# Performance work log

Hardware: AMD Instinct MI355X
Metric: run time of the kernel (lower is better)

Reference implementation:

```python
import jax, jax.numpy as jnp
import numpy as np

B, D, H, Z, E = 2048, 1024, 1024, 256, 64


def setup_inputs() -> dict:
    key = jax.random.key(0)
    ks = jax.random.split(key, 16)
    s = lambda k, shape, std=0.02: jax.random.normal(k, shape, dtype=jnp.float32) * std
    return {
        "x": jax.random.normal(ks[0], (B, D), dtype=jnp.float32),
        "h0": jax.random.normal(ks[1], (B, H), dtype=jnp.float32),
        "c0": jax.random.normal(ks[2], (B, H), dtype=jnp.float32),
        "hhat0": jax.random.normal(ks[3], (B, Z), dtype=jnp.float32),
        "chat0": jax.random.normal(ks[4], (B, Z), dtype=jnp.float32),
        "hweight": s(ks[5], (Z + H + D, 4 * Z)),
        "hbias": jnp.zeros((4 * Z,), jnp.float32),
        "zweight_h": s(ks[6], (Z, 4 * E), 0.01),
        "zweight_x": s(ks[7], (Z, 4 * E), 0.01),
        "zweight_b": s(ks[8], (Z, 4 * E), 0.01),
        "zbias_h": jnp.ones((4 * E,), jnp.float32),
        "zbias_x": jnp.ones((4 * E,), jnp.float32),
        # stacked in gate order (i, g, f, o), matching the torch cat order
        "dweight_h": jnp.full((4, E, H), 0.1 / E, jnp.float32),
        "dweight_x": jnp.full((4, E, H), 0.1 / E, jnp.float32),
        "dweight_b": s(ks[9], (4, E, H), 0.01),
        "weight": s(ks[10], (H + D, 4 * H)),
        "bias": jnp.zeros((4 * H,), jnp.float32),
    }


def reference(x, h0, c0, hhat0, chat0, hweight, hbias,
              zweight_h, zweight_x, zweight_b, zbias_h, zbias_x,
              dweight_h, dweight_x, dweight_b, weight, bias):
    # ---- hyper LSTM cell ----
    hcat = jnp.concatenate([hhat0, h0, x], axis=1)                 # [B, Z+H+D]
    hg = hcat @ hweight + hbias                                    # [B, 4Z]
    i_h, g_h, f_h, o_h = jnp.split(hg, 4, axis=1)
    chat1 = jax.nn.sigmoid(f_h) * chat0 + jax.nn.sigmoid(i_h) * jnp.tanh(g_h)
    hhat1 = jax.nn.sigmoid(o_h) * jnp.tanh(chat1)                  # [B, Z]

    # ---- embeddings z (gate order i, g, f, o) ----
    z_h = (hhat1 @ zweight_h + zbias_h).reshape(-1, 4, E)          # [B,4,E]
    z_x = (hhat1 @ zweight_x + zbias_x).reshape(-1, 4, E)
    z_b = (hhat1 @ zweight_b).reshape(-1, 4, E)

    # ---- per-gate modulation vectors d_y* : [B,4,H] -> [B,4H] ----
    d_yh = jnp.einsum('bge,geh->bgh', z_h, dweight_h).reshape(-1, 4 * H)
    d_yx = jnp.einsum('bge,geh->bgh', z_x, dweight_x).reshape(-1, 4 * H)
    d_yb = jnp.einsum('bge,geh->bgh', z_b, dweight_b).reshape(-1, 4 * H)

    # ---- main LSTM with hypernetwork modulation ----
    gates = jnp.concatenate([h0, x], axis=1) @ weight              # [B, 4H]
    gates = gates * d_yh * d_yx + d_yb + bias
    i_g, g_g, f_g, o_g = jnp.split(gates, 4, axis=1)
    c1 = jax.nn.sigmoid(f_g) * c0 + jax.nn.sigmoid(i_g) * jnp.tanh(g_g)
    h1 = jax.nn.sigmoid(o_g) * jnp.tanh(c1)
    return (h1, c1, hhat1, chat1)
```

## Files before the change

### kernel.cpp

```cpp
#include <hip/hip_runtime.h>
#include <hip/hip_bf16.h>
#include <math.h>


typedef __attribute__((ext_vector_type(8))) short bf16x8;
typedef __attribute__((ext_vector_type(4))) float f32x4;
typedef unsigned short u16;

__device__ __forceinline__ u16 f2b(float f) {
  union { float f; unsigned u; } v; v.f = f;
  unsigned r = v.u + 0x7fffu + ((v.u >> 16) & 1u);
  return (u16)(r >> 16);
}
__device__ __forceinline__ float b2f(u16 b) {
  union { unsigned u; float f; } v; v.u = ((unsigned)b) << 16; return v.f;
}
__device__ __forceinline__ float sigm(float x) { return 1.f / (1.f + __expf(-x)); }

#define GLL16(gsrc, ldst)                                                      \
  __builtin_amdgcn_global_load_lds(                                            \
      (const __attribute__((address_space(1))) void*)(gsrc),                   \
      (__attribute__((address_space(3))) void*)(ldst), 16, 0, 0)

__global__ void k_prep(const float* __restrict__ hhat0, const float* __restrict__ h0,
                       const float* __restrict__ x, const float* __restrict__ weight,
                       const float* __restrict__ hweight,
                       const float* __restrict__ zw_h, const float* __restrict__ zw_x,
                       const float* __restrict__ zw_b, const float* __restrict__ dw_h,
                       const float* __restrict__ dw_x, const float* __restrict__ dw_b,
                       u16* __restrict__ hcatb, u16* __restrict__ bt,
                       u16* __restrict__ zwT, u16* __restrict__ dwT) {
  __shared__ float tile[32][66];
  int bid = blockIdx.x;
  const int t = threadIdx.x;
  if (bid < 4608) {
    int i = bid * 256 + t;
    int b = i / 576, c4 = i % 576;
    const float* src;
    if (c4 < 64)       src = hhat0 + (long)b * 256 + c4 * 4;
    else if (c4 < 320) src = h0 + (long)b * 1024 + (c4 - 64) * 4;
    else               src = x + (long)b * 1024 + (c4 - 320) * 4;
    float4 v = *(const float4*)src;
    ushort4 o = {f2b(v.x), f2b(v.y), f2b(v.z), f2b(v.w)};
    *(ushort4*)&hcatb[(long)b * 2304 + c4 * 4] = o;
    return;
  }
  bid -= 4608;
  if (bid < 5760) {
    const int n0 = (bid % 160) * 32, k0 = (bid / 160) * 64;
    if (n0 < 4096 && k0 < 256) return;
    const float* src; int C, sc0, sr0;
    if (n0 >= 4096) { src = hweight; C = 1024; sc0 = n0 - 4096; sr0 = k0; }
    else            { src = weight;  C = 4096; sc0 = n0;        sr0 = k0 - 256; }
    #pragma unroll
    for (int p = 0; p < 8; ++p) {
      int c = t & 31, r = (t >> 5) + 8 * p;
      tile[c][r] = src[(long)(sr0 + r) * C + sc0 + c];
    }
    __syncthreads();
    #pragma unroll
    for (int p = 0; p < 2; ++p) {
      int kc = t & 15, cl = (t >> 4) + 16 * p;
      ushort4 o = {f2b(tile[cl][4 * kc]), f2b(tile[cl][4 * kc + 1]),
                   f2b(tile[cl][4 * kc + 2]), f2b(tile[cl][4 * kc + 3])};
      *(ushort4*)&bt[(long)(n0 + cl) * 2304 + k0 + 4 * kc] = o;
    }
    return;
  }
  bid -= 5760;
  const int zi = bid >> 5, bx = bid & 31;
  const float* src; u16* dst; int R, C;
  if (zi < 3) {
    src = (zi == 0) ? zw_h : (zi == 1) ? zw_x : zw_b;
    dst = zwT + (long)zi * 65536; R = 256; C = 256;
  } else {
    int s = zi - 3, tt = s >> 2, g = s & 3;
    src = ((tt == 0) ? dw_h : (tt == 1) ? dw_x : dw_b) + (long)g * 65536;
    dst = dwT + (long)s * 65536; R = 64; C = 1024;
  }
  const int nct = C / 32;
  const int c0 = (bx % nct) * 32, r0 = (bx / nct) * 64;
  #pragma unroll
  for (int p = 0; p < 8; ++p) {
    int c = t & 31, r = (t >> 5) + 8 * p;
    tile[c][r] = src[(long)(r0 + r) * C + c0 + c];
  }
  __syncthreads();
  #pragma unroll
  for (int p = 0; p < 2; ++p) {
    int kc = t & 15, cl = (t >> 4) + 16 * p;
    ushort4 o = {f2b(tile[cl][4 * kc]), f2b(tile[cl][4 * kc + 1]),
                 f2b(tile[cl][4 * kc + 2]), f2b(tile[cl][4 * kc + 3])};
    *(ushort4*)&dst[(long)(c0 + cl) * R + r0 + 4 * kc] = o;
  }
}

__global__ __launch_bounds__(512, 4)
void k_gemm_main(const u16* __restrict__ A, const u16* __restrict__ Bt,
                 float* __restrict__ hgbuf, u16* __restrict__ grawb) {
  constexpr int K = 2304, BK = 32;
  __shared__ __align__(16) u16 sA[128 * BK];
  __shared__ __align__(16) u16 sB[128 * BK];
  const int m0 = blockIdx.y * 128, n0 = blockIdx.x * 128;
  const int kstart = (n0 < 4096) ? 256 : 0;
  const int tid = threadIdx.x, wave = tid >> 6, lane = tid & 63;
  const int quad = lane >> 4, lrow = lane & 15;
  const int wm = (wave >> 2) * 64, wn = (wave & 3) * 32;

  const int sl = tid * 16;
  const int srow = sl >> 6;
  const int sq = (((sl & 63) >> 4) - (srow >> 1)) & 3;
  const long aoff = ((long)(m0 + srow) * K) * 2 + sq * 16;
  const long boff = ((long)(n0 + srow) * K) * 2 + sq * 16;

  const f32x4 vz = {0.f, 0.f, 0.f, 0.f};
  f32x4 acc[4][2];
  #pragma unroll
  for (int i = 0; i < 4; ++i)
    #pragma unroll
    for (int j = 0; j < 2; ++j) acc[i][j] = vz;

  for (int k0 = kstart; k0 < K; k0 += BK) {
    GLL16((const char*)A + aoff + (long)k0 * 2, (char*)sA + wave * 1024);
    GLL16((const char*)Bt + boff + (long)k0 * 2, (char*)sB + wave * 1024);
    __syncthreads();
    bf16x8 af[4], bf[2];
    #pragma unroll
    for (int i = 0; i < 4; ++i) {
      int row = wm + i * 16 + lrow;
      af[i] = *(const bf16x8*)((const char*)sA + row * 64 + (((quad + (row >> 1)) & 3) << 4));
    }
    #pragma unroll
    for (int j = 0; j < 2; ++j) {
      int row = wn + j * 16 + lrow;
      bf[j] = *(const bf16x8*)((const char*)sB + row * 64 + (((quad + (row >> 1)) & 3) << 4));
    }
    #pragma unroll
    for (int i = 0; i < 4; ++i)
      #pragma unroll
      for (int j = 0; j < 2; ++j)
        acc[i][j] = __builtin_amdgcn_mfma_f32_16x16x32_bf16(af[i], bf[j], acc[i][j], 0, 0, 0);
    __syncthreads();
  }
  #pragma unroll
  for (int i = 0; i < 4; ++i) {
    #pragma unroll
    for (int j = 0; j < 2; ++j) {
      #pragma unroll
      for (int r = 0; r < 4; ++r) {
        int row = m0 + wm + i * 16 + quad * 4 + r;
        int col = n0 + wn + j * 16 + lrow;
        float v = acc[i][j][r];
        if (col < 4096) grawb[(long)row * 4096 + col] = f2b(v);
        else            hgbuf[(long)row * 1024 + (col - 4096)] = v;
      }
    }
  }
}

__global__ __launch_bounds__(256, 2)
void k_gemm_z(const u16* __restrict__ A, const u16* __restrict__ Bt,
              const float* __restrict__ zbh, const float* __restrict__ zbx,
              u16* __restrict__ zbout) {
  constexpr int K = 256, BK = 32;
  __shared__ __align__(16) u16 sA[64 * BK];
  __shared__ __align__(16) u16 sB[128 * BK];
  const int m0 = blockIdx.y * 64, n0 = blockIdx.x * 128;
  const int tid = threadIdx.x, wave = tid >> 6, lane = tid & 63;
  const int quad = lane >> 4, lrow = lane & 15;
  const int wm = (wave >> 1) * 32, wn = (wave & 1) * 64;

  const int sl = tid * 16;
  const int arow = sl >> 6;
  const int aq = (((sl & 63) >> 4) - (arow >> 1)) & 3;
  const long aoff = ((long)(m0 + arow) * K) * 2 + aq * 16;

  const f32x4 vz = {0.f, 0.f, 0.f, 0.f};
  f32x4 acc[2][4];
  #pragma unroll
  for (int i = 0; i < 2; ++i)
    #pragma unroll
    for (int j = 0; j < 4; ++j) acc[i][j] = vz;

  for (int k0 = 0; k0 < K; k0 += BK) {
    GLL16((const char*)A + aoff + (long)k0 * 2, (char*)sA + wave * 1024);
    #pragma unroll
    for (int c = 0; c < 2; ++c) {
      int l = c * 4096 + sl;
      int row = l >> 6;
      int q = (((l & 63) >> 4) - (row >> 1)) & 3;
      const char* g = (const char*)Bt + ((long)(n0 + row) * K + k0) * 2 + q * 16;
      GLL16(g, (char*)sB + c * 4096 + wave * 1024);
    }
    __syncthreads();
    bf16x8 af[2], bf[4];
    #pragma unroll
    for (int i = 0; i < 2; ++i) {
      int row = wm + i * 16 + lrow;
      af[i] = *(const bf16x8*)((const char*)sA + row * 64 + (((quad + (row >> 1)) & 3) << 4));
    }
    #pragma unroll
    for (int j = 0; j < 4; ++j) {
      int row = wn + j * 16 + lrow;
      bf[j] = *(const bf16x8*)((const char*)sB + row * 64 + (((quad + (row >> 1)) & 3) << 4));
    }
    #pragma unroll
    for (int i = 0; i < 2; ++i)
      #pragma unroll
      for (int j = 0; j < 4; ++j)
        acc[i][j] = __builtin_amdgcn_mfma_f32_16x16x32_bf16(af[i], bf[j], acc[i][j], 0, 0, 0);
    __syncthreads();
  }
  #pragma unroll
  for (int i = 0; i < 2; ++i) {
    #pragma unroll
    for (int j = 0; j < 4; ++j) {
      #pragma unroll
      for (int r = 0; r < 4; ++r) {
        int row = m0 + wm + i * 16 + quad * 4 + r;
        int col = n0 + wn + j * 16 + lrow;
        float v = acc[i][j][r] + ((col < 256) ? zbh[col] : (col < 512) ? zbx[col - 256] : 0.f);
        zbout[(long)row * 768 + col] = f2b(v);
      }
    }
  }
}

__global__ void k_hyper_act(const float* __restrict__ hgbuf, const float* __restrict__ hbias,
                            const float* __restrict__ chat0,
                            float* __restrict__ chat1, float* __restrict__ hhat1,
                            u16* __restrict__ hhat1b) {
  int idx = blockIdx.x * 256 + threadIdx.x;
  int b = idx >> 8, zc = idx & 255;
  const float* row = hgbuf + (long)b * 1024;
  float ih = row[zc] + hbias[zc];
  float gh = row[256 + zc] + hbias[256 + zc];
  float fh = row[512 + zc] + hbias[512 + zc];
  float oh = row[768 + zc] + hbias[768 + zc];
  float c = sigm(fh) * chat0[idx] + sigm(ih) * tanhf(gh);
  float h = sigm(oh) * tanhf(c);
  chat1[idx] = c;
  hhat1[idx] = h;
  hhat1b[idx] = f2b(h);
}

__global__ __launch_bounds__(256, 2)
void k_dmod_lstm(const u16* __restrict__ z, const u16* __restrict__ dwT,
                 const u16* __restrict__ grawb, const float* __restrict__ bias,
                 const float* __restrict__ c0, float* __restrict__ h1,
                 float* __restrict__ c1) {
  __shared__ __align__(16) u16 sZ[64 * 192];
  __shared__ __align__(16) u16 sW[3 * 64 * 64];
  const int m0 = blockIdx.y * 64;
  const int hc0 = blockIdx.x * 64;
  const int tid = threadIdx.x, wave = tid >> 6, lane = tid & 63;
  const int quad = lane >> 4, lrow = lane & 15;
  const int wm = (wave >> 1) * 32, wn = (wave & 1) * 32;
  const f32x4 vz4 = {0.f, 0.f, 0.f, 0.f};

  f32x4 pcar[2][2];
  f32x4 ccar[2][2];

  #pragma unroll
  for (int g = 0; g < 4; ++g) {
    #pragma unroll
    for (int c = 0; c < 6; ++c) {
      int l = c * 4096 + tid * 16;
      int ci = l >> 4, row = ci / 24, p = ci - row * 24;
      int q = p + 72 - row; q -= (q / 24) * 24;
      int tt = q >> 3, e16 = q & 7;
      const char* gz = (const char*)z + (long)(m0 + row) * 1536 + tt * 512 + g * 128 + e16 * 16;
      GLL16(gz, (char*)sZ + c * 4096 + wave * 1024);
      int t2 = l >> 13, rw = (l & 8191) >> 7, p2 = (l >> 4) & 7;
      int q2 = (p2 - rw) & 7;
      const char* gw = (const char*)dwT + (long)((t2 * 4 + g) * 1024 + hc0 + rw) * 128 + q2 * 16;
      GLL16(gw, (char*)sW + c * 4096 + wave * 1024);
    }
    __syncthreads();
    f32x4 aH[2][2], aX[2][2], aB[2][2];
    #pragma unroll
    for (int i = 0; i < 2; ++i)
      #pragma unroll
      for (int j = 0; j < 2; ++j) { aH[i][j] = vz4; aX[i][j] = vz4; aB[i][j] = vz4; }
    #pragma unroll
    for (int kk = 0; kk < 2; ++kk) {
      bf16x8 za[3][2], wb[3][2];
      #pragma unroll
      for (int t = 0; t < 3; ++t) {
        #pragma unroll
        for (int i = 0; i < 2; ++i) {
          int row = wm + i * 16 + lrow;
          int q0 = t * 8 + kk * 4 + quad;
          int ph = q0 + row; ph -= (ph / 24) * 24;
          za[t][i] = *(const bf16x8*)((const char*)sZ + row * 384 + ph * 16);
        }
        #pragma unroll
        for (int j = 0; j < 2; ++j) {
          int row = wn + j * 16 + lrow;
          int q0 = kk * 4 + quad;
          int ph = (q0 + row) & 7;
          wb[t][j] = *(const bf16x8*)((const char*)sW + t * 8192 + row * 128 + ph * 16);
        }
      }
      #pragma unroll
      for (int i = 0; i < 2; ++i)
        #pragma unroll
        for (int j = 0; j < 2; ++j) {
          aH[i][j] = __builtin_amdgcn_mfma_f32_16x16x32_bf16(za[0][i], wb[0][j], aH[i][j], 0, 0, 0);
          aX[i][j] = __builtin_amdgcn_mfma_f32_16x16x32_bf16(za[1][i], wb[1][j], aX[i][j], 0, 0, 0);
          aB[i][j] = __builtin_amdgcn_mfma_f32_16x16x32_bf16(za[2][i], wb[2][j], aB[i][j], 0, 0, 0);
        }
    }
    __syncthreads();
    #pragma unroll
    for (int i = 0; i < 2; ++i) {
      #pragma unroll
      for (int j = 0; j < 2; ++j) {
        #pragma unroll
        for (int r = 0; r < 4; ++r) {
          int row = m0 + wm + i * 16 + quad * 4 + r;
          int col = wn + j * 16 + lrow;
          float gr = b2f(grawb[(long)row * 4096 + g * 1024 + hc0 + col]);
          float v = gr * aH[i][j][r] * aX[i][j][r] + aB[i][j][r] + bias[g * 1024 + hc0 + col];
          long idx = (long)row * 1024 + hc0 + col;
          if (g == 0) pcar[i][j][r] = sigm(v);
          else if (g == 1) pcar[i][j][r] *= tanhf(v);
          else if (g == 2) {
            float cc = sigm(v) * c0[idx] + pcar[i][j][r];
            ccar[i][j][r] = cc;
            c1[idx] = cc;
          } else {
            h1[idx] = sigm(v) * tanhf(ccar[i][j][r]);
          }
        }
      }
    }
  }
}


extern "C" void kernel_launch(void* const* d_in, const int* in_sizes, int n_in,
                              void* d_out, int out_size, void* d_ws, size_t ws_size,
                              hipStream_t stream) {
  const float* x      = (const float*)d_in[0];
  const float* h0     = (const float*)d_in[1];
  const float* c0     = (const float*)d_in[2];
  const float* hhat0  = (const float*)d_in[3];
  const float* chat0  = (const float*)d_in[4];
  const float* hweight= (const float*)d_in[5];
  const float* hbias  = (const float*)d_in[6];
  const float* zw_h   = (const float*)d_in[7];
  const float* zw_x   = (const float*)d_in[8];
  const float* zw_b   = (const float*)d_in[9];
  const float* zb_h   = (const float*)d_in[10];
  const float* zb_x   = (const float*)d_in[11];
  const float* dw_h   = (const float*)d_in[12];
  const float* dw_x   = (const float*)d_in[13];
  const float* dw_b   = (const float*)d_in[14];
  const float* weight = (const float*)d_in[15];
  const float* bias   = (const float*)d_in[16];
  float* out = (float*)d_out;

  char* w = (char*)d_ws;
  auto take = [&](size_t bytes) { char* p = w; w += (bytes + 255) & ~(size_t)255; return p; };
  u16*   hcatb  = (u16*)take(2048ull * 2304 * 2);
  u16*   btc    = (u16*)take(5120ull * 2304 * 2);
  u16*   zwT    = (u16*)take(768ull * 256 * 2);
  u16*   dwT    = (u16*)take(12ull * 1024 * 64 * 2);
  u16*   grawb  = (u16*)take(2048ull * 4096 * 2);
  float* hgbuf  = (float*)take(2048ull * 1024 * 4);
  u16*   hhat1b = (u16*)take(2048ull * 256 * 2);
  u16*   zb16   = (u16*)take(2048ull * 768 * 2);

  float* h1_o    = out;
  float* c1_o    = out + 2048 * 1024;
  float* hhat1_o = out + 2 * 2048 * 1024;
  float* chat1_o = out + 2 * 2048 * 1024 + 2048 * 256;

  k_prep<<<4608 + 5760 + 480, 256, 0, stream>>>(
      hhat0, h0, x, weight, hweight, zw_h, zw_x, zw_b, dw_h, dw_x, dw_b,
      hcatb, btc, zwT, dwT);

  k_gemm_main<<<dim3(40, 16), 512, 0, stream>>>(hcatb, btc, hgbuf, grawb);

  k_hyper_act<<<2048, 256, 0, stream>>>(hgbuf, hbias, chat0, chat1_o, hhat1_o, hhat1b);

  k_gemm_z<<<dim3(6, 32), 256, 0, stream>>>(hhat1b, zwT, zb_h, zb_x, zb16);

  k_dmod_lstm<<<dim3(16, 32), 256, 0, stream>>>(zb16, dwT, grawb, bias, c0, h1_o, c1_o);
}
```

Before: 230.8 us.

## Widen main GEMM K-tile, fuse hyper cell into z GEMM, drop LDS in dmod

The main GEMM now stages a 64-wide K slice per iteration with an 8-way XOR swizzle, which halves the number of barrier-separated loop trips. The hyper-LSTM activation kernel is folded into the z GEMM: each block computes hhat1 for its 64 rows straight into LDS, so the separate launch and the bf16 hhat1 round trip go away. Six column blocks each recompute the same rows, which duplicates the transcendental work. The dmod/LSTM kernel no longer stages z and dW through shared memory and loads MFMA operands directly from global memory, removing barriers but relying on cache hits for reuse.

After: 273.3 us. +18.4%, slower.

```diff
diff --git a/kernel.cpp b/kernel.cpp
--- a/kernel.cpp
+++ b/kernel.cpp
@@ -98,20 +98,23 @@
 __global__ __launch_bounds__(512, 4)
 void k_gemm_main(const u16* __restrict__ A, const u16* __restrict__ Bt,
                  float* __restrict__ hgbuf, u16* __restrict__ grawb) {
-  constexpr int K = 2304, BK = 32;
-  __shared__ __align__(16) u16 sA[128 * BK];
-  __shared__ __align__(16) u16 sB[128 * BK];
+  constexpr int K = 2304;
+  __shared__ __align__(16) u16 sA[128 * 64];
+  __shared__ __align__(16) u16 sB[128 * 64];
   const int m0 = blockIdx.y * 128, n0 = blockIdx.x * 128;
   const int kstart = (n0 < 4096) ? 256 : 0;
   const int tid = threadIdx.x, wave = tid >> 6, lane = tid & 63;
   const int quad = lane >> 4, lrow = lane & 15;
   const int wm = (wave >> 2) * 64, wn = (wave & 3) * 32;
 
-  const int sl = tid * 16;
-  const int srow = sl >> 6;
-  const int sq = (((sl & 63) >> 4) - (srow >> 1)) & 3;
-  const long aoff = ((long)(m0 + srow) * K) * 2 + sq * 16;
-  const long boff = ((long)(n0 + srow) * K) * 2 + sq * 16;
+  const int l0 = tid * 16, l1 = 8192 + tid * 16;
+  const int r0 = l0 >> 7, r1 = l1 >> 7;
+  const int q0 = (((l0 >> 4) & 7) - r0) & 7;
+  const int q1 = (((l1 >> 4) & 7) - r1) & 7;
+  const long aoff0 = ((long)(m0 + r0) * K + q0 * 8) * 2;
+  const long aoff1 = ((long)(m0 + r1) * K + q1 * 8) * 2;
+  const long boff0 = ((long)(n0 + r0) * K + q0 * 8) * 2;
+  const long boff1 = ((long)(n0 + r1) * K + q1 * 8) * 2;
 
   const f32x4 vz = {0.f, 0.f, 0.f, 0.f};
   f32x4 acc[4][2];
@@ -120,26 +123,34 @@
     #pragma unroll
     for (int j = 0; j < 2; ++j) acc[i][j] = vz;
 
-  for (int k0 = kstart; k0 < K; k0 += BK) {
-    GLL16((const char*)A + aoff + (long)k0 * 2, (char*)sA + wave * 1024);
-    GLL16((const char*)Bt + boff + (long)k0 * 2, (char*)sB + wave * 1024);
-    __syncthreads();
-    bf16x8 af[4], bf[2];
-    #pragma unroll
-    for (int i = 0; i < 4; ++i) {
-      int row = wm + i * 16 + lrow;
-      af[i] = *(const bf16x8*)((const char*)sA + row * 64 + (((quad + (row >> 1)) & 3) << 4));
-    }
-    #pragma unroll
-    for (int j = 0; j < 2; ++j) {
-      int row = wn + j * 16 + lrow;
-      bf[j] = *(const bf16x8*)((const char*)sB + row * 64 + (((quad + (row >> 1)) & 3) << 4));
-    }
-    #pragma unroll
-    for (int i = 0; i < 4; ++i)
-      #pragma unroll
-      for (int j = 0; j < 2; ++j)
-        acc[i][j] = __builtin_amdgcn_mfma_f32_16x16x32_bf16(af[i], bf[j], acc[i][j], 0, 0, 0);
+  for (int k0 = kstart; k0 < K; k0 += 64) {
+    const long kb = (long)k0 * 2;
+    GLL16((const char*)A + aoff0 + kb, (char*)sA + wave * 1024);
+    GLL16((const char*)A + aoff1 + kb, (char*)sA + 8192 + wave * 1024);
+    GLL16((const char*)Bt + boff0 + kb, (char*)sB + wave * 1024);
+    GLL16((const char*)Bt + boff1 + kb, (char*)sB + 8192 + wave * 1024);
+    __syncthreads();
+    #pragma unroll
+    for (int kk = 0; kk < 2; ++kk) {
+      bf16x8 af[4], bf[2];
+      #pragma unroll
+      for (int i = 0; i < 4; ++i) {
+        int row = wm + i * 16 + lrow;
+        int ph = (kk * 4 + quad + row) & 7;
+        af[i] = *(const bf16x8*)((const char*)sA + row * 128 + ph * 16);
+      }
+      #pragma unroll
+      for (int j = 0; j < 2; ++j) {
+        int row = wn + j * 16 + lrow;
+        int ph = (kk * 4 + quad + row) & 7;
+        bf[j] = *(const bf16x8*)((const char*)sB + row * 128 + ph * 16);
+      }
+      #pragma unroll
+      for (int i = 0; i < 4; ++i)
+        #pragma unroll
+        for (int j = 0; j < 2; ++j)
+          acc[i][j] = __builtin_amdgcn_mfma_f32_16x16x32_bf16(af[i], bf[j], acc[i][j], 0, 0, 0);
+    }
     __syncthreads();
   }
   #pragma unroll
@@ -159,22 +170,38 @@
 }
 
 __global__ __launch_bounds__(256, 2)
-void k_gemm_z(const u16* __restrict__ A, const u16* __restrict__ Bt,
-              const float* __restrict__ zbh, const float* __restrict__ zbx,
-              u16* __restrict__ zbout) {
-  constexpr int K = 256, BK = 32;
-  __shared__ __align__(16) u16 sA[64 * BK];
-  __shared__ __align__(16) u16 sB[128 * BK];
+void k_gemm_zcell(const float* __restrict__ hg, const float* __restrict__ hbias,
+                  const float* __restrict__ chat0, const u16* __restrict__ zwT,
+                  const float* __restrict__ zbh, const float* __restrict__ zbx,
+                  float* __restrict__ chat1, float* __restrict__ hhat1,
+                  u16* __restrict__ zbout) {
+  __shared__ __align__(16) u16 sH[64 * 256];
+  __shared__ __align__(16) u16 sB[128 * 32];
   const int m0 = blockIdx.y * 64, n0 = blockIdx.x * 128;
-  const int tid = threadIdx.x, wave = tid >> 6, lane = tid & 63;
+  const int tid = threadIdx.x;
+
+  {
+    const int zc = tid;
+    const float hb_i = hbias[zc], hb_g = hbias[256 + zc];
+    const float hb_f = hbias[512 + zc], hb_o = hbias[768 + zc];
+    #pragma unroll 4
+    for (int row = 0; row < 64; ++row) {
+      const float* r = hg + (long)(m0 + row) * 1024;
+      float ih = r[zc] + hb_i, gh = r[256 + zc] + hb_g;
+      float fh = r[512 + zc] + hb_f, oh = r[768 + zc] + hb_o;
+      long cidx = (long)(m0 + row) * 256 + zc;
+      float c = sigm(fh) * chat0[cidx] + sigm(ih) * tanhf(gh);
+      float h = sigm(oh) * tanhf(c);
+      if (n0 == 0) { chat1[cidx] = c; hhat1[cidx] = h; }
+      int ph = ((zc >> 3) + row) & 31;
+      sH[row * 256 + ph * 8 + (zc & 7)] = f2b(h);
+    }
+  }
+  __syncthreads();
+
+  const int wave = tid >> 6, lane = tid & 63;
   const int quad = lane >> 4, lrow = lane & 15;
   const int wm = (wave >> 1) * 32, wn = (wave & 1) * 64;
-
-  const int sl = tid * 16;
-  const int arow = sl >> 6;
-  const int aq = (((sl & 63) >> 4) - (arow >> 1)) & 3;
-  const long aoff = ((long)(m0 + arow) * K) * 2 + aq * 16;
-
   const f32x4 vz = {0.f, 0.f, 0.f, 0.f};
   f32x4 acc[2][4];
   #pragma unroll
@@ -182,14 +209,13 @@
     #pragma unroll
     for (int j = 0; j < 4; ++j) acc[i][j] = vz;
 
-  for (int k0 = 0; k0 < K; k0 += BK) {
-    GLL16((const char*)A + aoff + (long)k0 * 2, (char*)sA + wave * 1024);
+  for (int k0 = 0; k0 < 256; k0 += 32) {
     #pragma unroll
     for (int c = 0; c < 2; ++c) {
-      int l = c * 4096 + sl;
+      int l = c * 4096 + tid * 16;
       int row = l >> 6;
-      int q = (((l & 63) >> 4) - (row >> 1)) & 3;
-      const char* g = (const char*)Bt + ((long)(n0 + row) * K + k0) * 2 + q * 16;
+      int q = (((l >> 4) & 3) - (row >> 1)) & 3;
+      const char* g = (const char*)zwT + ((long)(n0 + row) * 256 + k0 + q * 8) * 2;
       GLL16(g, (char*)sB + c * 4096 + wave * 1024);
     }
     __syncthreads();
@@ -197,12 +223,14 @@
     #pragma unroll
     for (int i = 0; i < 2; ++i) {
       int row = wm + i * 16 + lrow;
-      af[i] = *(const bf16x8*)((const char*)sA + row * 64 + (((quad + (row >> 1)) & 3) << 4));
+      int ph = ((k0 >> 3) + quad + row) & 31;
+      af[i] = *(const bf16x8*)((const char*)sH + row * 512 + ph * 16);
     }
     #pragma unroll
     for (int j = 0; j < 4; ++j) {
       int row = wn + j * 16 + lrow;
-      bf[j] = *(const bf16x8*)((const char*)sB + row * 64 + (((quad + (row >> 1)) & 3) << 4));
+      int ph = (quad + (row >> 1)) & 3;
+      bf[j] = *(const bf16x8*)((const char*)sB + row * 64 + ph * 16);
     }
     #pragma unroll
     for (int i = 0; i < 2; ++i)
@@ -226,36 +254,16 @@
   }
 }
 
-__global__ void k_hyper_act(const float* __restrict__ hgbuf, const float* __restrict__ hbias,
-                            const float* __restrict__ chat0,
-                            float* __restrict__ chat1, float* __restrict__ hhat1,
-                            u16* __restrict__ hhat1b) {
-  int idx = blockIdx.x * 256 + threadIdx.x;
-  int b = idx >> 8, zc = idx & 255;
-  const float* row = hgbuf + (long)b * 1024;
-  float ih = row[zc] + hbias[zc];
-  float gh = row[256 + zc] + hbias[256 + zc];
-  float fh = row[512 + zc] + hbias[512 + zc];
-  float oh = row[768 + zc] + hbias[768 + zc];
-  float c = sigm(fh) * chat0[idx] + sigm(ih) * tanhf(gh);
-  float h = sigm(oh) * tanhf(c);
-  chat1[idx] = c;
-  hhat1[idx] = h;
-  hhat1b[idx] = f2b(h);
-}
-
 __global__ __launch_bounds__(256, 2)
 void k_dmod_lstm(const u16* __restrict__ z, const u16* __restrict__ dwT,
                  const u16* __restrict__ grawb, const float* __restrict__ bias,
                  const float* __restrict__ c0, float* __restrict__ h1,
                  float* __restrict__ c1) {
-  __shared__ __align__(16) u16 sZ[64 * 192];
-  __shared__ __align__(16) u16 sW[3 * 64 * 64];
-  const int m0 = blockIdx.y * 64;
-  const int hc0 = blockIdx.x * 64;
+  const int m0 = blockIdx.y * 64, hc0 = blockIdx.x * 64;
   const int tid = threadIdx.x, wave = tid >> 6, lane = tid & 63;
   const int quad = lane >> 4, lrow = lane & 15;
-  const int wm = (wave >> 1) * 32, wn = (wave & 1) * 32;
+  const int rm = m0 + (wave >> 1) * 32;
+  const int cn = hc0 + (wave & 1) * 32;
   const f32x4 vz4 = {0.f, 0.f, 0.f, 0.f};
 
   f32x4 pcar[2][2];
@@ -263,66 +271,51 @@
 
   #pragma unroll
   for (int g = 0; g < 4; ++g) {
-    #pragma unroll
-    for (int c = 0; c < 6; ++c) {
-      int l = c * 4096 + tid * 16;
-      int ci = l >> 4, row = ci / 24, p = ci - row * 24;
-      int q = p + 72 - row; q -= (q / 24) * 24;
-      int tt = q >> 3, e16 = q & 7;
-      const char* gz = (const char*)z + (long)(m0 + row) * 1536 + tt * 512 + g * 128 + e16 * 16;
-      GLL16(gz, (char*)sZ + c * 4096 + wave * 1024);
-      int t2 = l >> 13, rw = (l & 8191) >> 7, p2 = (l >> 4) & 7;
-      int q2 = (p2 - rw) & 7;
-      const char* gw = (const char*)dwT + (long)((t2 * 4 + g) * 1024 + hc0 + rw) * 128 + q2 * 16;
-      GLL16(gw, (char*)sW + c * 4096 + wave * 1024);
-    }
-    __syncthreads();
     f32x4 aH[2][2], aX[2][2], aB[2][2];
     #pragma unroll
     for (int i = 0; i < 2; ++i)
       #pragma unroll
       for (int j = 0; j < 2; ++j) { aH[i][j] = vz4; aX[i][j] = vz4; aB[i][j] = vz4; }
-    #pragma unroll
-    for (int kk = 0; kk < 2; ++kk) {
-      bf16x8 za[3][2], wb[3][2];
-      #pragma unroll
-      for (int t = 0; t < 3; ++t) {
-        #pragma unroll
-        for (int i = 0; i < 2; ++i) {
-          int row = wm + i * 16 + lrow;
-          int q0 = t * 8 + kk * 4 + quad;
-          int ph = q0 + row; ph -= (ph / 24) * 24;
-          za[t][i] = *(const bf16x8*)((const char*)sZ + row * 384 + ph * 16);
-        }
-        #pragma unroll
-        for (int j = 0; j < 2; ++j) {
-          int row = wn + j * 16 + lrow;
-          int q0 = kk * 4 + quad;
-          int ph = (q0 + row) & 7;
-          wb[t][j] = *(const bf16x8*)((const char*)sW + t * 8192 + row * 128 + ph * 16);
-        }
-      }
-      #pragma unroll
-      for (int i = 0; i < 2; ++i)
-        #pragma unroll
-        for (int j = 0; j < 2; ++j) {
-          aH[i][j] = __builtin_amdgcn_mfma_f32_16x16x32_bf16(za[0][i], wb[0][j], aH[i][j], 0, 0, 0);
-          aX[i][j] = __builtin_amdgcn_mfma_f32_16x16x32_bf16(za[1][i], wb[1][j], aX[i][j], 0, 0, 0);
-          aB[i][j] = __builtin_amdgcn_mfma_f32_16x16x32_bf16(za[2][i], wb[2][j], aB[i][j], 0, 0, 0);
-        }
-    }
-    __syncthreads();
+
+    #pragma unroll
+    for (int t = 0; t < 3; ++t) {
+      bf16x8 za[2][2], wb[2][2];
+      #pragma unroll
+      for (int kk = 0; kk < 2; ++kk) {
+        #pragma unroll
+        for (int i = 0; i < 2; ++i)
+          za[kk][i] = *(const bf16x8*)(z + (long)(rm + i * 16 + lrow) * 768 +
+                                       t * 256 + g * 64 + kk * 32 + quad * 8);
+        #pragma unroll
+        for (int j = 0; j < 2; ++j)
+          wb[kk][j] = *(const bf16x8*)(dwT + (long)((t * 4 + g) * 1024 + cn + j * 16 + lrow) * 64 +
+                                       kk * 32 + quad * 8);
+      }
+      #pragma unroll
+      for (int kk = 0; kk < 2; ++kk)
+        #pragma unroll
+        for (int i = 0; i < 2; ++i)
+          #pragma unroll
+          for (int j = 0; j < 2; ++j) {
+            if (t == 0)
+              aH[i][j] = __builtin_amdgcn_mfma_f32_16x16x32_bf16(za[kk][i], wb[kk][j], aH[i][j], 0, 0, 0);
+            else if (t == 1)
+              aX[i][j] = __builtin_amdgcn_mfma_f32_16x16x32_bf16(za[kk][i], wb[kk][j], aX[i][j], 0, 0, 0);
+            else
+              aB[i][j] = __builtin_amdgcn_mfma_f32_16x16x32_bf16(za[kk][i], wb[kk][j], aB[i][j], 0, 0, 0);
+          }
+    }
     #pragma unroll
     for (int i = 0; i < 2; ++i) {
       #pragma unroll
       for (int j = 0; j < 2; ++j) {
         #pragma unroll
         for (int r = 0; r < 4; ++r) {
-          int row = m0 + wm + i * 16 + quad * 4 + r;
-          int col = wn + j * 16 + lrow;
-          float gr = b2f(grawb[(long)row * 4096 + g * 1024 + hc0 + col]);
-          float v = gr * aH[i][j][r] * aX[i][j][r] + aB[i][j][r] + bias[g * 1024 + hc0 + col];
-          long idx = (long)row * 1024 + hc0 + col;
+          int row = rm + i * 16 + quad * 4 + r;
+          int col = cn + j * 16 + lrow;
+          float gr = b2f(grawb[(long)row * 4096 + g * 1024 + col]);
+          float v = gr * aH[i][j][r] * aX[i][j][r] + aB[i][j][r] + bias[g * 1024 + col];
+          long idx = (long)row * 1024 + col;
           if (g == 0) pcar[i][j][r] = sigm(v);
           else if (g == 1) pcar[i][j][r] *= tanhf(v);
           else if (g == 2) {
@@ -369,7 +362,6 @@
   u16*   dwT    = (u16*)take(12ull * 1024 * 64 * 2);
   u16*   grawb  = (u16*)take(2048ull * 4096 * 2);
   float* hgbuf  = (float*)take(2048ull * 1024 * 4);
-  u16*   hhat1b = (u16*)take(2048ull * 256 * 2);
   u16*   zb16   = (u16*)take(2048ull * 768 * 2);
 
   float* h1_o    = out;
@@ -383,9 +375,8 @@
 
   k_gemm_main<<<dim3(40, 16), 512, 0, stream>>>(hcatb, btc, hgbuf, grawb);
 
-  k_hyper_act<<<2048, 256, 0, stream>>>(hgbuf, hbias, chat0, chat1_o, hhat1_o, hhat1b);
-
-  k_gemm_z<<<dim3(6, 32), 256, 0, stream>>>(hhat1b, zwT, zb_h, zb_x, zb16);
+  k_gemm_zcell<<<dim3(6, 32), 256, 0, stream>>>(hgbuf, hbias, chat0, zwT, zb_h, zb_x,
+                                                chat1_o, hhat1_o, zb16);
 
   k_dmod_lstm<<<dim3(16, 32), 256, 0, stream>>>(zb16, dwT, grawb, bias, c0, h1_o, c1_o);
 }
```
